# Kernel optimization log

Measured on AMD Instinct MI355X. Metric: run time of the kernel, lower is better.

## Reference

```python
import jax, jax.numpy as jnp
import numpy as np

DIM = 512
HEADS = 8
TOP_K = 16


def setup_inputs() -> dict:
    key = jax.random.key(0)
    ks = jax.random.split(key, 7)
    B, N, C = 8, 1024, DIM
    std = 0.02
    return {
        "x": jax.random.normal(ks[0], (B, N, C), dtype=jnp.float32),
        "Wq": jax.random.normal(ks[1], (C, C), dtype=jnp.float32) * std,
        "bq": jnp.zeros((C,), dtype=jnp.float32),
        "Wkv": jax.random.normal(ks[2], (C, 2 * C), dtype=jnp.float32) * std,
        "bkv": jnp.zeros((2 * C,), dtype=jnp.float32),
        "Wp": jax.random.normal(ks[3], (C, C), dtype=jnp.float32) * std,
        "bp": jnp.zeros((C,), dtype=jnp.float32),
    }


def reference(x, Wq, bq, Wkv, bkv, Wp, bp):
    B, N, C = x.shape
    H = HEADS
    D = C // H
    scale = D ** (-0.5)

    # q: [B,H,N,D], ReLU-activated
    q = (x @ Wq + bq).reshape(B, N, H, D).transpose(0, 2, 1, 3)
    q = jax.nn.relu(q)
    # kv: [B,N,2,H,D] -> k,v each [B,H,N,D]
    kv = (x @ Wkv + bkv).reshape(B, N, 2, H, D).transpose(2, 0, 3, 1, 4)
    k, v = kv[0], kv[1]

    # dense scores [B,H,N,N]
    attn = jnp.einsum('bhnd,bhmd->bhnm', q, k) * scale

    # top-k mask along last dim (scatter ones at topk indices)
    _, idx = jax.lax.top_k(attn, TOP_K)            # [B,H,N,K]
    flat_attn = attn.reshape(-1, N)
    flat_idx = idx.reshape(-1, TOP_K)
    rows = jnp.arange(flat_attn.shape[0])[:, None]
    mask = jnp.zeros_like(flat_attn).at[rows, flat_idx].set(1.0).reshape(attn.shape)

    # NOTE: faithful to the original - softmax over the full row of attn*mask
    # (masked-out entries contribute exp(0)=1, exactly as in the torch code)
    sparse_attn = jax.nn.softmax(attn * mask, axis=-1)

    out = jnp.einsum('bhnm,bhmd->bhnd', sparse_attn, v)
    out = out.transpose(0, 2, 1, 3).reshape(B, N, C)
    out = out @ Wp + bp
    return out
```

## Files before the change

### kernel.cpp

```cpp
#include <hip/hip_runtime.h>
#include <float.h>

#define BATCH 8
#define SEQ   1024
#define CDIM  512
#define HEADS 8
#define HD    64
#define TOPK  16
#define MTOT  (BATCH*SEQ)

typedef short bf16x8 __attribute__((ext_vector_type(8)));
typedef float f32x4v __attribute__((ext_vector_type(4)));
typedef unsigned int __attribute__((address_space(1))) guint;
typedef unsigned int __attribute__((address_space(3))) luint;

__device__ inline void bf16split(float f, unsigned short& h, unsigned short& l) {
    unsigned u = __float_as_uint(f);
    unsigned hr = (u + 0x7fffu + ((u >> 16) & 1u)) >> 16;
    h = (unsigned short)hr;
    float rest = f - __uint_as_float(hr << 16);
    unsigned v = __float_as_uint(rest);
    l = (unsigned short)((v + 0x7fffu + ((v >> 16) & 1u)) >> 16);
}

__global__ __launch_bounds__(256) void split_x_kernel(
    const float* __restrict__ x,
    unsigned short* __restrict__ xhi, unsigned short* __restrict__ xlo)
{
    size_t i = ((size_t)blockIdx.x * 256 + threadIdx.x) * 4;
    float4 v = *(const float4*)(x + i);
    ushort4 h, l;
    bf16split(v.x, h.x, l.x); bf16split(v.y, h.y, l.y);
    bf16split(v.z, h.z, l.z); bf16split(v.w, h.w, l.w);
    *(ushort4*)(xhi + i) = h;
    *(ushort4*)(xlo + i) = l;
}

__global__ __launch_bounds__(256) void split_wT_kernel(
    const float* __restrict__ Wq, const float* __restrict__ Wkv,
    const float* __restrict__ Wp,
    unsigned short* __restrict__ bThi, unsigned short* __restrict__ bTlo,
    unsigned short* __restrict__ wpThi, unsigned short* __restrict__ wpTlo)
{
    __shared__ float tile[64][65];
    const int ct = blockIdx.x, k0 = blockIdx.y * 64, t = threadIdx.x;
    const float* src; int ld, sc0, dr0;
    unsigned short *dhi, *dlo;
    if (ct < 8)       { src = Wq;  ld = CDIM;     sc0 = ct * 64;        dr0 = ct * 64;              dhi = bThi;  dlo = bTlo;  }
    else if (ct < 24) { src = Wkv; ld = 2 * CDIM; sc0 = (ct - 8) * 64;  dr0 = CDIM + (ct - 8) * 64; dhi = bThi;  dlo = bTlo;  }
    else              { src = Wp;  ld = CDIM;     sc0 = (ct - 24) * 64; dr0 = (ct - 24) * 64;       dhi = wpThi; dlo = wpTlo; }

    #pragma unroll
    for (int i = 0; i < 4; i++) {
        int f = t + i * 256;
        int r = f >> 4, c4 = f & 15;
        float4 v = *(const float4*)(src + (size_t)(k0 + r) * ld + sc0 + c4 * 4);
        tile[c4*4+0][r] = v.x; tile[c4*4+1][r] = v.y;
        tile[c4*4+2][r] = v.z; tile[c4*4+3][r] = v.w;
    }
    __syncthreads();
    #pragma unroll
    for (int i = 0; i < 2; i++) {
        int f = t + i * 256;
        int c = f >> 3, ko = f & 7;
        const float* tp = &tile[c][ko * 8];
        ushort4 h0, l0, h1, l1;
        bf16split(tp[0], h0.x, l0.x); bf16split(tp[1], h0.y, l0.y);
        bf16split(tp[2], h0.z, l0.z); bf16split(tp[3], h0.w, l0.w);
        bf16split(tp[4], h1.x, l1.x); bf16split(tp[5], h1.y, l1.y);
        bf16split(tp[6], h1.z, l1.z); bf16split(tp[7], h1.w, l1.w);
        size_t o = (size_t)(dr0 + c) * CDIM + k0 + ko * 8;
        *(ushort4*)(dhi + o)     = h0; *(ushort4*)(dhi + o + 4) = h1;
        *(ushort4*)(dlo + o)     = l0; *(ushort4*)(dlo + o + 4) = l1;
    }
}

__device__ __forceinline__ void mfma_gemm_core8(
    const unsigned short* __restrict__ ahi, const unsigned short* __restrict__ alo,
    const unsigned short* __restrict__ bhi, const unsigned short* __restrict__ blo,
    int row0, int col0, int lane, int w, f32x4v acc[2][4])
{
    __shared__ __align__(16) unsigned short ah_s[2][4096], al_s[2][4096];
    __shared__ __align__(16) unsigned short bh_s[2][4096], bl_s[2][4096];

    const int op = w >> 1;
    const int ch0 = (w & 1) * 4;
    const unsigned short* gsrc;
    unsigned short* lb[2];
    if (op == 0)      { gsrc = ahi; lb[0] = ah_s[0]; lb[1] = ah_s[1]; }
    else if (op == 1) { gsrc = alo; lb[0] = al_s[0]; lb[1] = al_s[1]; }
    else if (op == 2) { gsrc = bhi; lb[0] = bh_s[0]; lb[1] = bh_s[1]; }
    else              { gsrc = blo; lb[0] = bl_s[0]; lb[1] = bl_s[1]; }
    const int tile0 = (op < 2) ? row0 : col0;
    const size_t goff = (size_t)(tile0 + (lane & 15)) * CDIM + (lane >> 4) * 8;

    const int rowg = w >> 1;
    const int colg = w & 1;

    #pragma unroll
    for (int i = 0; i < 2; i++)
        #pragma unroll
        for (int j = 0; j < 4; j++)
            acc[i][j] = (f32x4v){0.f, 0.f, 0.f, 0.f};

    #pragma unroll
    for (int cc = 0; cc < 4; cc++)
        __builtin_amdgcn_global_load_lds(
            (const guint*)(gsrc + goff + (size_t)(ch0 + cc) * 16 * CDIM),
            (luint*)(lb[0] + (ch0 + cc) * 512), 16, 0, 0);
    asm volatile("s_waitcnt vmcnt(0)" ::: "memory");
    __builtin_amdgcn_s_barrier();

    int cur = 0;
    for (int kt = 0; kt < CDIM; kt += 32) {
        if (kt + 32 < CDIM) {
            unsigned short* ln = lb[cur ^ 1];
            #pragma unroll
            for (int cc = 0; cc < 4; cc++)
                __builtin_amdgcn_global_load_lds(
                    (const guint*)(gsrc + goff + kt + 32 + (size_t)(ch0 + cc) * 16 * CDIM),
                    (luint*)(ln + (ch0 + cc) * 512), 16, 0, 0);
        }

        const unsigned short* ah = ah_s[cur];
        const unsigned short* al = al_s[cur];
        const unsigned short* bh = bh_s[cur];
        const unsigned short* bl = bl_s[cur];
        bf16x8 afh[2], afl[2], bfh[4], bfl[4];
        #pragma unroll
        for (int i = 0; i < 2; i++) {
            afh[i] = *(const bf16x8*)&ah[(((rowg*2 + i) * 64) + lane) * 8];
            afl[i] = *(const bf16x8*)&al[(((rowg*2 + i) * 64) + lane) * 8];
        }
        #pragma unroll
        for (int j = 0; j < 4; j++) {
            bfh[j] = *(const bf16x8*)&bh[(((colg*4 + j) * 64) + lane) * 8];
            bfl[j] = *(const bf16x8*)&bl[(((colg*4 + j) * 64) + lane) * 8];
        }
        #pragma unroll
        for (int i = 0; i < 2; i++)
            #pragma unroll
            for (int j = 0; j < 4; j++) {
                acc[i][j] = __builtin_amdgcn_mfma_f32_16x16x32_bf16(bfh[j], afh[i], acc[i][j], 0, 0, 0);
                acc[i][j] = __builtin_amdgcn_mfma_f32_16x16x32_bf16(bfh[j], afl[i], acc[i][j], 0, 0, 0);
                acc[i][j] = __builtin_amdgcn_mfma_f32_16x16x32_bf16(bfl[j], afh[i], acc[i][j], 0, 0, 0);
            }

        __builtin_amdgcn_sched_barrier(0);
        asm volatile("s_waitcnt vmcnt(0)" ::: "memory");
        __builtin_amdgcn_s_barrier();
        cur ^= 1;
    }
}

__global__ __launch_bounds__(512) void qkv_mfma_kernel(
    const unsigned short* __restrict__ xhi, const unsigned short* __restrict__ xlo,
    const unsigned short* __restrict__ bThi, const unsigned short* __restrict__ bTlo,
    const float* __restrict__ bq, const float* __restrict__ bkv,
    unsigned short* __restrict__ qhi_g, unsigned short* __restrict__ qlo_g,
    unsigned short* __restrict__ khi_g, unsigned short* __restrict__ klo_g,
    float* __restrict__ v_ws)
{
    const int tid = threadIdx.x, lane = tid & 63, w = tid >> 6;
    const int row0 = blockIdx.x * 128, col0 = blockIdx.y * 128;

    f32x4v acc[2][4];
    mfma_gemm_core8(xhi, xlo, bThi, bTlo, row0, col0, lane, w, acc);

    const int rowg = w >> 1, colg = w & 1;
    const bool isq = (col0 < CDIM);
    #pragma unroll
    for (int i = 0; i < 2; i++) {
        int rG = row0 + (rowg*2 + i) * 16 + (lane & 15);
        int bb = rG >> 10, nn = rG & (SEQ - 1);
        #pragma unroll
        for (int j = 0; j < 4; j++) {
            int cG = col0 + (colg*4 + j) * 16 + (lane >> 4) * 4;
            float4 bias4 = isq ? *(const float4*)(bq + cG)
                               : *(const float4*)(bkv + cG - CDIM);
            float4 val;
            val.x = acc[i][j][0] + bias4.x;
            val.y = acc[i][j][1] + bias4.y;
            val.z = acc[i][j][2] + bias4.z;
            val.w = acc[i][j][3] + bias4.w;
            if (isq) {
                val.x = fmaxf(val.x, 0.f); val.y = fmaxf(val.y, 0.f);
                val.z = fmaxf(val.z, 0.f); val.w = fmaxf(val.w, 0.f);
                int hq = cG >> 6, d = cG & 63;
                size_t base = (((size_t)bb * HEADS + hq) * SEQ + nn) * HD + d;
                ushort4 hv, lv;
                bf16split(val.x, hv.x, lv.x); bf16split(val.y, hv.y, lv.y);
                bf16split(val.z, hv.z, lv.z); bf16split(val.w, hv.w, lv.w);
                *(ushort4*)(qhi_g + base) = hv;
                *(ushort4*)(qlo_g + base) = lv;
            } else {
                int c2 = cG - CDIM;
                int t = c2 >> 9, hq = (c2 >> 6) & 7, d = c2 & 63;
                size_t base = (((size_t)bb * HEADS + hq) * SEQ + nn) * HD + d;
                if (t == 0) {
                    ushort4 hv, lv;
                    bf16split(val.x, hv.x, lv.x); bf16split(val.y, hv.y, lv.y);
                    bf16split(val.z, hv.z, lv.z); bf16split(val.w, hv.w, lv.w);
                    *(ushort4*)(khi_g + base) = hv;
                    *(ushort4*)(klo_g + base) = lv;
                } else {
                    *(float4*)(v_ws + base) = val;
                }
            }
        }
    }
}

__global__ __launch_bounds__(256) void vsum_kernel(
    const float* __restrict__ v_ws, float* __restrict__ vsum_ws)
{
    __shared__ float red[4][HD];
    const int bh = blockIdx.x;
    const int d  = threadIdx.x & 63;
    const int sl = threadIdx.x >> 6;
    const float* vh = v_ws + (size_t)bh * SEQ * HD;
    float s = 0.f;
    for (int m = sl * 256; m < (sl + 1) * 256; m++) s += vh[(size_t)m * HD + d];
    red[sl][d] = s;
    __syncthreads();
    if (threadIdx.x < HD)
        vsum_ws[(size_t)bh * HD + d] = red[0][d] + red[1][d] + red[2][d] + red[3][d];
}

__global__ __launch_bounds__(256) void score_kernel(
    const unsigned short* __restrict__ qhi_g, const unsigned short* __restrict__ qlo_g,
    const unsigned short* __restrict__ khi_g, const unsigned short* __restrict__ klo_g,
    float* __restrict__ s_g, int bh0)
{
    __shared__ __align__(16) short qhi_s[4096], qlo_s[4096];
    __shared__ __align__(16) short khi_s[2][4096], klo_s[2][4096];

    const int bhl = blockIdx.y;
    const int bh  = bh0 + bhl;
    const int n0  = blockIdx.x * 64;
    const int tid = threadIdx.x;
    const int lane = tid & 63, w = tid >> 6;
    const int r_st = tid >> 2, c4 = tid & 3;
    const size_t hb = (size_t)bh * SEQ * HD;

    const int s0 = c4 * 2, s1 = s0 + 1;
    const int cx0 = ((r_st >> 4)*2 + (s0 >> 2))*64 + (s0 & 3)*16 + (r_st & 15);
    const int cx1 = ((r_st >> 4)*2 + (s1 >> 2))*64 + (s1 & 3)*16 + (r_st & 15);

    {
        const unsigned short* qp  = qhi_g + hb + (size_t)(n0 + r_st)*HD + c4*16;
        const unsigned short* qp2 = qlo_g + hb + (size_t)(n0 + r_st)*HD + c4*16;
        uint4 h0 = *(const uint4*)qp,  h1 = *(const uint4*)(qp + 8);
        uint4 l0 = *(const uint4*)qp2, l1 = *(const uint4*)(qp2 + 8);
        *(uint4*)&qhi_s[cx0*8] = h0; *(uint4*)&qhi_s[cx1*8] = h1;
        *(uint4*)&qlo_s[cx0*8] = l0; *(uint4*)&qlo_s[cx1*8] = l1;
    }
    __syncthreads();
    bf16x8 qh[2], ql[2];
    #pragma unroll
    for (int h = 0; h < 2; h++) {
        qh[h] = *(bf16x8*)&qhi_s[((w*2 + h)*64 + lane)*8];
        ql[h] = *(bf16x8*)&qlo_s[((w*2 + h)*64 + lane)*8];
    }

    {
        const unsigned short* kp  = khi_g + hb + (size_t)r_st*HD + c4*16;
        const unsigned short* kp2 = klo_g + hb + (size_t)r_st*HD + c4*16;
        uint4 kh0 = *(const uint4*)kp,  kh1 = *(const uint4*)(kp + 8);
        uint4 kl0 = *(const uint4*)kp2, kl1 = *(const uint4*)(kp2 + 8);
        *(uint4*)&khi_s[0][cx0*8] = kh0; *(uint4*)&khi_s[0][cx1*8] = kh1;
        *(uint4*)&klo_s[0][cx0*8] = kl0; *(uint4*)&klo_s[0][cx1*8] = kl1;
    }
    __syncthreads();

    float* srow_base = s_g + ((size_t)bhl << 20);

    for (int mt = 0; mt < SEQ / 64; mt++) {
        const int cur = mt & 1, nxt = cur ^ 1;
        uint4 kh0, kh1, kl0, kl1;
        if (mt + 1 < SEQ / 64) {
            const unsigned short* kp  = khi_g + hb + (size_t)((mt+1)*64 + r_st)*HD + c4*16;
            const unsigned short* kp2 = klo_g + hb + (size_t)((mt+1)*64 + r_st)*HD + c4*16;
            kh0 = *(const uint4*)kp;  kh1 = *(const uint4*)(kp + 8);
            kl0 = *(const uint4*)kp2; kl1 = *(const uint4*)(kp2 + 8);
        }

        #pragma unroll
        for (int ct = 0; ct < 4; ct++) {
            f32x4v acc = {0.f, 0.f, 0.f, 0.f};
            #pragma unroll
            for (int h = 0; h < 2; h++) {
                bf16x8 kfh = *(bf16x8*)&khi_s[cur][((ct*2 + h)*64 + lane)*8];
                bf16x8 kfl = *(bf16x8*)&klo_s[cur][((ct*2 + h)*64 + lane)*8];
                acc = __builtin_amdgcn_mfma_f32_16x16x32_bf16(qh[h], kfh, acc, 0, 0, 0);
                acc = __builtin_amdgcn_mfma_f32_16x16x32_bf16(qh[h], kfl, acc, 0, 0, 0);
                acc = __builtin_amdgcn_mfma_f32_16x16x32_bf16(ql[h], kfh, acc, 0, 0, 0);
            }
            const int col  = mt*64 + ct*16 + (lane & 15);
            const int rowb = n0 + w*16 + (lane >> 4)*4;
            float* sp = srow_base + ((size_t)rowb << 10) + col;
            #pragma unroll
            for (int rg = 0; rg < 4; rg++)
                sp[(size_t)rg << 10] = acc[rg] * 0.125f;
        }

        if (mt + 1 < SEQ / 64) {
            *(uint4*)&khi_s[nxt][cx0*8] = kh0; *(uint4*)&khi_s[nxt][cx1*8] = kh1;
            *(uint4*)&klo_s[nxt][cx0*8] = kl0; *(uint4*)&klo_s[nxt][cx1*8] = kl1;
        }
        __syncthreads();
    }
}

__device__ __forceinline__ unsigned long long packkey(float f, int gidx) {
    unsigned u = __float_as_uint(f);
    unsigned o = u ^ ((unsigned)((int)u >> 31) | 0x80000000u);
    return ((unsigned long long)o << 32) | (unsigned)(~gidx);
}

struct TopCache { unsigned long long t0, t1, t2, t3; int cnt; };

__device__ __forceinline__ void cache_insert(TopCache& c, unsigned long long k) {
    bool b0 = k > c.t0, b1 = k > c.t1, b2 = k > c.t2, b3 = k > c.t3;
    c.t3 = b3 ? (b2 ? c.t2 : k) : c.t3;
    c.t2 = b2 ? (b1 ? c.t1 : k) : c.t2;
    c.t1 = b1 ? (b0 ? c.t0 : k) : c.t1;
    c.t0 = b0 ? k : c.t0;
}

__device__ __forceinline__ void cache_build(TopCache& c, const float* v, int gbase) {
    c.t0 = c.t1 = c.t2 = c.t3 = 0ull;
    #pragma unroll
    for (int j = 0; j < 16; j++) cache_insert(c, packkey(v[j], gbase + j));
    c.cnt = 4;
}

__device__ __forceinline__ void cache_pop_own(TopCache& c, bool own) {
    c.t0 = own ? c.t1 : c.t0;
    c.t1 = own ? c.t2 : c.t1;
    c.t2 = own ? c.t3 : c.t2;
    c.t3 = own ? 0ull : c.t3;
    c.cnt -= own;
}

__device__ __forceinline__ void cache_refill(TopCache& c, const float* v,
                                             int gbase, unsigned long long kw) {
    c.t0 = c.t1 = c.t2 = c.t3 = 0ull;
    int cc = 0;
    #pragma unroll
    for (int j = 0; j < 16; j++) {
        unsigned long long k = packkey(v[j], gbase + j);
        if (k < kw) { cc++; cache_insert(c, k); }
    }
    c.cnt = cc > 4 ? 4 : cc;
}

__device__ __forceinline__ unsigned umax2(unsigned a, unsigned b) { return a > b ? a : b; }

__device__ __forceinline__ unsigned wave_max_ord(unsigned o) {
    unsigned p;
    p = (unsigned)__builtin_amdgcn_update_dpp(0, (int)o, 0xB1, 0xF, 0xF, true); o = umax2(o, p);
    p = (unsigned)__builtin_amdgcn_update_dpp(0, (int)o, 0x4E, 0xF, 0xF, true); o = umax2(o, p);
    p = (unsigned)__builtin_amdgcn_ds_swizzle((int)o, 0x101F); o = umax2(o, p);
    p = (unsigned)__builtin_amdgcn_ds_swizzle((int)o, 0x201F); o = umax2(o, p);
    p = (unsigned)__builtin_amdgcn_ds_swizzle((int)o, 0x401F); o = umax2(o, p);
    p = (unsigned)__shfl_xor((int)o, 32);                      o = umax2(o, p);
    return o;
}

__device__ __forceinline__ float ord_to_float(unsigned o) {
    return __uint_as_float(o ^ ((unsigned)((int)(~o) >> 31) | 0x80000000u));
}

__global__ __launch_bounds__(256) void topk_pv_kernel(
    const float* __restrict__ s_g, const float* __restrict__ v_ws,
    const float* __restrict__ vsum_ws,
    unsigned short* __restrict__ aohi, unsigned short* __restrict__ aolo, int bh0)
{
    __shared__ unsigned pair_s[4][TOPK][2];

    const int lane = threadIdx.x & 63;
    const int wv   = threadIdx.x >> 6;
    const int wid  = (blockIdx.x * 256 + threadIdx.x) >> 6;
    const int bhl  = wid >> 10;
    const int n    = wid & (SEQ - 1);
    const int bh   = bh0 + bhl;
    const int gbase = lane * 16;

    const float* srow = s_g + ((size_t)bhl << 20) + ((size_t)n << 10) + gbase;
    float v[16];
    #pragma unroll
    for (int i = 0; i < 4; i++) {
        float4 t4 = *(const float4*)(srow + i * 4);
        v[i*4+0] = t4.x; v[i*4+1] = t4.y; v[i*4+2] = t4.z; v[i*4+3] = t4.w;
    }

    TopCache c;
    cache_build(c, v, gbase);

    float mx, e, Z;

    {
        unsigned o = (unsigned)(c.t0 >> 32);
        unsigned m = wave_max_ord(o);
        unsigned long long bl = __ballot(o == m);
        int s = __ffsll(bl) - 1;
        unsigned lo = (unsigned)__builtin_amdgcn_readlane((int)(unsigned)c.t0, s);
        float val = ord_to_float(m);

        mx = fmaxf(val, 0.f);
        e  = __expf(-mx);
        float wE = __expf(val - mx);
        Z = (float)(SEQ - TOPK) * e + wE;
        if (lane == 0) {
            pair_s[wv][0][0] = __float_as_uint(wE);
            pair_s[wv][0][1] = (~lo) & 1023u;
        }
        cache_pop_own(c, lane == s);
    }

    #pragma unroll 1
    for (int t = 1; t < TOPK; t++) {
        unsigned o = (unsigned)(c.t0 >> 32);
        unsigned m = wave_max_ord(o);
        unsigned long long bl = __ballot(o == m);
        int s = __ffsll(bl) - 1;
        unsigned lo = (unsigned)__builtin_amdgcn_readlane((int)(unsigned)c.t0, s);
        float val = ord_to_float(m);

        float wE = __expf(val - mx);
        Z += wE;
        if (lane == 0) {
            pair_s[wv][t][0] = __float_as_uint(wE);
            pair_s[wv][t][1] = (~lo) & 1023u;
        }
        cache_pop_own(c, lane == s);

        if (c.cnt == 0 && t < TOPK - 1) {
            unsigned long long kw = ((unsigned long long)m << 32) | lo;
            cache_refill(c, v, gbase, kw);
        }
    }

    float wexp[TOPK]; int mi[TOPK];
    #pragma unroll
    for (int t = 0; t < TOPK; t++) {
        wexp[t] = __uint_as_float(pair_s[wv][t][0]);
        mi[t]   = (int)pair_s[wv][t][1];
    }
    const float* vhp = v_ws + ((size_t)bh << 16);
    float vr[TOPK];
    #pragma unroll
    for (int t = 0; t < TOPK; t++)
        vr[t] = vhp[((size_t)mi[t] << 6) + lane];

    float acc = e * vsum_ws[(bh << 6) + lane];
    #pragma unroll
    for (int t = 0; t < TOPK; t++)
        acc = fmaf(wexp[t] - e, vr[t], acc);
    acc /= Z;

    const int b = bh >> 3, hh = bh & 7;
    size_t oo = (((size_t)b << 10) + n) * CDIM + (hh << 6) + lane;
    unsigned short sh, sl;
    bf16split(acc, sh, sl);
    aohi[oo] = sh;
    aolo[oo] = sl;
}

__global__ __launch_bounds__(512) void proj_mfma_kernel(
    const unsigned short* __restrict__ aohi, const unsigned short* __restrict__ aolo,
    const unsigned short* __restrict__ wpThi, const unsigned short* __restrict__ wpTlo,
    const float* __restrict__ bp, float* __restrict__ out)
{
    const int tid = threadIdx.x, lane = tid & 63, w = tid >> 6;
    const int row0 = blockIdx.x * 128, col0 = blockIdx.y * 128;

    f32x4v acc[2][4];
    mfma_gemm_core8(aohi, aolo, wpThi, wpTlo, row0, col0, lane, w, acc);

    const int rowg = w >> 1, colg = w & 1;
    #pragma unroll
    for (int i = 0; i < 2; i++) {
        int rG = row0 + (rowg*2 + i) * 16 + (lane & 15);
        #pragma unroll
        for (int j = 0; j < 4; j++) {
            int cG = col0 + (colg*4 + j) * 16 + (lane >> 4) * 4;
            float4 b4 = *(const float4*)(bp + cG);
            float4 val;
            val.x = acc[i][j][0] + b4.x;
            val.y = acc[i][j][1] + b4.y;
            val.z = acc[i][j][2] + b4.z;
            val.w = acc[i][j][3] + b4.w;
            *(float4*)(out + (size_t)rG * CDIM + cG) = val;
        }
    }
}

extern "C" void kernel_launch(void* const* d_in, const int* in_sizes, int n_in,
                              void* d_out, int out_size, void* d_ws, size_t ws_size,
                              hipStream_t stream)
{
    const float* x   = (const float*)d_in[0];
    const float* Wq  = (const float*)d_in[1];
    const float* bq  = (const float*)d_in[2];
    const float* Wkv = (const float*)d_in[3];
    const float* bkv = (const float*)d_in[4];
    const float* Wp  = (const float*)d_in[5];
    const float* bp  = (const float*)d_in[6];
    float* out = (float*)d_out;

    const size_t HSZ = (size_t)BATCH * HEADS * SEQ * HD;
    float* ws    = (float*)d_ws;
    float* v_ws  = ws;
    float* vs_ws = ws + HSZ;
    unsigned short* qhi_g = (unsigned short*)(ws + HSZ + 4096);
    unsigned short* qlo_g = qhi_g + HSZ;
    unsigned short* khi_g = qhi_g + 2 * HSZ;
    unsigned short* klo_g = qhi_g + 3 * HSZ;
    unsigned short* xhi_g = qhi_g + 4 * HSZ;
    unsigned short* xlo_g = qhi_g + 5 * HSZ;
    unsigned short* bThi  = qhi_g + 6 * HSZ;
    unsigned short* bTlo  = bThi + (size_t)1536 * 512;
    unsigned short* wpThi = bThi + (size_t)2 * 1536 * 512;
    unsigned short* wpTlo = wpThi + (size_t)512 * 512;

    const size_t plane_us = 6 * HSZ + (size_t)2 * 1536 * 512 + (size_t)2 * 512 * 512;
    const size_t base_fl  = HSZ + 4096 + plane_us / 2;
    float* s_g = ws + base_fl;

    const size_t avail_fl = (ws_size / 4 > base_fl) ? (ws_size / 4 - base_fl) : 0;
    int G = 32;
    while (G > 1 && (size_t)G * SEQ * SEQ > avail_fl) G >>= 1;

    split_x_kernel<<<dim3((MTOT * CDIM) / (256 * 4)), 256, 0, stream>>>(x, xhi_g, xlo_g);
    split_wT_kernel<<<dim3(32, 8), 256, 0, stream>>>(Wq, Wkv, Wp, bThi, bTlo, wpThi, wpTlo);
    qkv_mfma_kernel<<<dim3(MTOT / 128, 12), 512, 0, stream>>>(
        xhi_g, xlo_g, bThi, bTlo, bq, bkv, qhi_g, qlo_g, khi_g, klo_g, v_ws);
    vsum_kernel<<<BATCH * HEADS, 256, 0, stream>>>(v_ws, vs_ws);
    for (int bh0 = 0; bh0 < BATCH * HEADS; bh0 += G) {
        score_kernel<<<dim3(SEQ / 64, G), 256, 0, stream>>>(
            qhi_g, qlo_g, khi_g, klo_g, s_g, bh0);
        topk_pv_kernel<<<dim3(G * (SEQ / 4)), 256, 0, stream>>>(
            s_g, v_ws, vs_ws, xhi_g, xlo_g, bh0);
    }
    proj_mfma_kernel<<<dim3(MTOT / 128, CDIM / 128), 512, 0, stream>>>(
        xhi_g, xlo_g, wpThi, wpTlo, bp, out);
}
```

Measured before the change: 339.5 us.

## Load Q/K tiles directly to LDS and write transposed score tiles as float4

Replaces register-staged global-to-LDS copies in the score kernel with direct global_load_lds transfers, splitting the hi/lo planes across waves. The MFMA operands are swapped so each lane holds four consecutive columns of one row, letting score stores become a single float4 write instead of four strided scalar writes. Synchronisation is switched to explicit vmcnt waits plus s_barrier, which is meant to overlap the next K tile load with compute. The hand-counted vmcnt(4) must match the outstanding loads per wave, and the fixed row mapping of the direct-to-LDS writes has to reproduce the previous swizzled layout.

```diff
diff --git a/kernel.cpp b/kernel.cpp
--- a/kernel.cpp
+++ b/kernel.cpp
@@ -232,30 +232,39 @@
     const unsigned short* __restrict__ khi_g, const unsigned short* __restrict__ klo_g,
     float* __restrict__ s_g, int bh0)
 {
-    __shared__ __align__(16) short qhi_s[4096], qlo_s[4096];
-    __shared__ __align__(16) short khi_s[2][4096], klo_s[2][4096];
+    __shared__ __align__(16) unsigned short qhi_s[4096], qlo_s[4096];
+    __shared__ __align__(16) unsigned short khi_s[2][4096], klo_s[2][4096];
 
     const int bhl = blockIdx.y;
     const int bh  = bh0 + bhl;
     const int n0  = blockIdx.x * 64;
     const int tid = threadIdx.x;
     const int lane = tid & 63, w = tid >> 6;
-    const int r_st = tid >> 2, c4 = tid & 3;
     const size_t hb = (size_t)bh * SEQ * HD;
 
-    const int s0 = c4 * 2, s1 = s0 + 1;
-    const int cx0 = ((r_st >> 4)*2 + (s0 >> 2))*64 + (s0 & 3)*16 + (r_st & 15);
-    const int cx1 = ((r_st >> 4)*2 + (s1 >> 2))*64 + (s1 & 3)*16 + (r_st & 15);
-
-    {
-        const unsigned short* qp  = qhi_g + hb + (size_t)(n0 + r_st)*HD + c4*16;
-        const unsigned short* qp2 = qlo_g + hb + (size_t)(n0 + r_st)*HD + c4*16;
-        uint4 h0 = *(const uint4*)qp,  h1 = *(const uint4*)(qp + 8);
-        uint4 l0 = *(const uint4*)qp2, l1 = *(const uint4*)(qp2 + 8);
-        *(uint4*)&qhi_s[cx0*8] = h0; *(uint4*)&qhi_s[cx1*8] = h1;
-        *(uint4*)&qlo_s[cx0*8] = l0; *(uint4*)&qlo_s[cx1*8] = l1;
-    }
-    __syncthreads();
+    const int pl = w & 1;
+    const int cb = (w >> 1) * 4;
+    const unsigned short* qsrc = pl ? qlo_g : qhi_g;
+    const unsigned short* ksrc = pl ? klo_g : khi_g;
+    unsigned short* qdst = pl ? qlo_s : qhi_s;
+    unsigned short* kdst[2];
+    kdst[0] = pl ? klo_s[0] : khi_s[0];
+    kdst[1] = pl ? klo_s[1] : khi_s[1];
+
+    #pragma unroll
+    for (int cc = 0; cc < 4; cc++) {
+        int c = cb + cc;
+        size_t off = (size_t)((c >> 1) * 16 + (lane & 15)) * HD + (c & 1) * 32 + (lane >> 4) * 8;
+        __builtin_amdgcn_global_load_lds(
+            (const guint*)(qsrc + hb + (size_t)n0 * HD + off),
+            (luint*)(qdst + c * 512), 16, 0, 0);
+        __builtin_amdgcn_global_load_lds(
+            (const guint*)(ksrc + hb + off),
+            (luint*)(kdst[0] + c * 512), 16, 0, 0);
+    }
+    asm volatile("s_waitcnt vmcnt(0)" ::: "memory");
+    __builtin_amdgcn_s_barrier();
+
     bf16x8 qh[2], ql[2];
     #pragma unroll
     for (int h = 0; h < 2; h++) {
@@ -263,52 +272,48 @@
         ql[h] = *(bf16x8*)&qlo_s[((w*2 + h)*64 + lane)*8];
     }
 
-    {
-        const unsigned short* kp  = khi_g + hb + (size_t)r_st*HD + c4*16;
-        const unsigned short* kp2 = klo_g + hb + (size_t)r_st*HD + c4*16;
-        uint4 kh0 = *(const uint4*)kp,  kh1 = *(const uint4*)(kp + 8);
-        uint4 kl0 = *(const uint4*)kp2, kl1 = *(const uint4*)(kp2 + 8);
-        *(uint4*)&khi_s[0][cx0*8] = kh0; *(uint4*)&khi_s[0][cx1*8] = kh1;
-        *(uint4*)&klo_s[0][cx0*8] = kl0; *(uint4*)&klo_s[0][cx1*8] = kl1;
-    }
-    __syncthreads();
-
-    float* srow_base = s_g + ((size_t)bhl << 20);
-
+    const int qrow = n0 + w*16 + (lane & 15);
+    float* srow = s_g + ((size_t)bhl << 20) + ((size_t)qrow << 10) + (lane >> 4) * 4;
+
+    int cur = 0;
     for (int mt = 0; mt < SEQ / 64; mt++) {
-        const int cur = mt & 1, nxt = cur ^ 1;
-        uint4 kh0, kh1, kl0, kl1;
         if (mt + 1 < SEQ / 64) {
-            const unsigned short* kp  = khi_g + hb + (size_t)((mt+1)*64 + r_st)*HD + c4*16;
-            const unsigned short* kp2 = klo_g + hb + (size_t)((mt+1)*64 + r_st)*HD + c4*16;
-            kh0 = *(const uint4*)kp;  kh1 = *(const uint4*)(kp + 8);
-            kl0 = *(const uint4*)kp2; kl1 = *(const uint4*)(kp2 + 8);
-        }
-
+            unsigned short* kd = kdst[cur ^ 1];
+            #pragma unroll
+            for (int cc = 0; cc < 4; cc++) {
+                int c = cb + cc;
+                size_t off = (size_t)((c >> 1) * 16 + (lane & 15)) * HD + (c & 1) * 32 + (lane >> 4) * 8;
+                __builtin_amdgcn_global_load_lds(
+                    (const guint*)(ksrc + hb + (size_t)(mt + 1) * 64 * HD + off),
+                    (luint*)(kd + c * 512), 16, 0, 0);
+            }
+        }
+
+        const unsigned short* kh = khi_s[cur];
+        const unsigned short* kl = klo_s[cur];
         #pragma unroll
         for (int ct = 0; ct < 4; ct++) {
             f32x4v acc = {0.f, 0.f, 0.f, 0.f};
             #pragma unroll
             for (int h = 0; h < 2; h++) {
-                bf16x8 kfh = *(bf16x8*)&khi_s[cur][((ct*2 + h)*64 + lane)*8];
-                bf16x8 kfl = *(bf16x8*)&klo_s[cur][((ct*2 + h)*64 + lane)*8];
-                acc = __builtin_amdgcn_mfma_f32_16x16x32_bf16(qh[h], kfh, acc, 0, 0, 0);
-                acc = __builtin_amdgcn_mfma_f32_16x16x32_bf16(qh[h], kfl, acc, 0, 0, 0);
-                acc = __builtin_amdgcn_mfma_f32_16x16x32_bf16(ql[h], kfh, acc, 0, 0, 0);
+                bf16x8 kfh = *(const bf16x8*)&kh[((ct*2 + h)*64 + lane)*8];
+                bf16x8 kfl = *(const bf16x8*)&kl[((ct*2 + h)*64 + lane)*8];
+                acc = __builtin_amdgcn_mfma_f32_16x16x32_bf16(kfh, qh[h], acc, 0, 0, 0);
+                acc = __builtin_amdgcn_mfma_f32_16x16x32_bf16(kfl, qh[h], acc, 0, 0, 0);
+                acc = __builtin_amdgcn_mfma_f32_16x16x32_bf16(kfh, ql[h], acc, 0, 0, 0);
             }
-            const int col  = mt*64 + ct*16 + (lane & 15);
-            const int rowb = n0 + w*16 + (lane >> 4)*4;
-            float* sp = srow_base + ((size_t)rowb << 10) + col;
-            #pragma unroll
-            for (int rg = 0; rg < 4; rg++)
-                sp[(size_t)rg << 10] = acc[rg] * 0.125f;
+            float4 sv;
+            sv.x = acc[0] * 0.125f; sv.y = acc[1] * 0.125f;
+            sv.z = acc[2] * 0.125f; sv.w = acc[3] * 0.125f;
+            *(float4*)(srow + mt * 64 + ct * 16) = sv;
         }
 
         if (mt + 1 < SEQ / 64) {
-            *(uint4*)&khi_s[nxt][cx0*8] = kh0; *(uint4*)&khi_s[nxt][cx1*8] = kh1;
-            *(uint4*)&klo_s[nxt][cx0*8] = kl0; *(uint4*)&klo_s[nxt][cx1*8] = kl1;
-        }
-        __syncthreads();
+            __builtin_amdgcn_sched_barrier(0);
+            asm volatile("s_waitcnt vmcnt(4)" ::: "memory");
+            __builtin_amdgcn_s_barrier();
+        }
+        cur ^= 1;
     }
 }
 
```

Result: no change. 343.9 us (+1.3%).
